# Optimization experiments

Hardware: AMD Instinct MI355X
Metric: run time of the kernel (lower is better)

The kernel has to match this reference:

```python
import jax, jax.numpy as jnp
import numpy as np

S = 2048      # sequence length
D = 2048      # d_model
H = 16        # n_heads
E = 128       # d_head


def setup_inputs() -> dict:
    key = jax.random.key(0)
    kx, kw = jax.random.split(key)
    x = jax.random.normal(kx, (S, D), dtype=jnp.float32)
    # xavier_normal for fan_in=D, fan_out=3*E per head
    std = float(np.sqrt(2.0 / (D + 3 * E)))
    w_qkv = jax.random.normal(kw, (H, D, 3 * E), dtype=jnp.float32) * std
    return {"x": x, "w_qkv": w_qkv}


def reference(x, w_qkv):
    # qkv: [h, s, 3e]
    qkv = jnp.einsum('sd,hde->hse', x, w_qkv)
    q, k, v = jnp.split(qkv, 3, axis=-1)            # each [h, s, e]
    scores = jnp.einsum('hse,hte->hst', q, k) / jnp.sqrt(jnp.asarray(E, x.dtype))
    attn = jax.nn.softmax(scores, axis=-1)          # [h, s, t]
    out = jnp.einsum('hst,hte->hse', attn, v)       # [h, s, e]
    # concat heads: [s, h*e]
    return out.transpose(1, 0, 2).reshape(x.shape[0], -1)
```

## Files before the change

### kernel.cpp

```cpp
#include <hip/hip_runtime.h>

#define SEQ 2048
#define DMODEL 2048
#define NHEAD 16
#define EHEAD 128
#define NE3 384

using short8 = __attribute__((ext_vector_type(8))) short;
using f32x4  = __attribute__((ext_vector_type(4))) float;
using f32x16 = __attribute__((ext_vector_type(16))) float;
using uint4v = __attribute__((ext_vector_type(4))) unsigned int;

__device__ __forceinline__ unsigned short f32_to_bf16(float f) {
    unsigned int u = __float_as_uint(f);
    unsigned int rounding = 0x7fffu + ((u >> 16) & 1u);
    u += rounding;
    return (unsigned short)(u >> 16);
}

__device__ __forceinline__ void async_load16(const void* g, void* l) {
    __builtin_amdgcn_global_load_lds(
        (const __attribute__((address_space(1))) unsigned int*)g,
        (__attribute__((address_space(3))) unsigned int*)l, 16, 0, 0);
}

#define WG_BARRIER()                              \
    do {                                          \
        asm volatile("" ::: "memory");            \
        __builtin_amdgcn_s_barrier();             \
        asm volatile("" ::: "memory");            \
    } while (0)

__global__ void cast_x_kernel(const float* __restrict__ x, unsigned short* __restrict__ xb) {
    int i = (blockIdx.x * blockDim.x + threadIdx.x) * 4;
    float4 v = *(const float4*)(x + i);
    ushort4 o = make_ushort4(f32_to_bf16(v.x), f32_to_bf16(v.y), f32_to_bf16(v.z), f32_to_bf16(v.w));
    *(ushort4*)(xb + i) = o;
}

__global__ void transpose_w_kernel(const float* __restrict__ w, unsigned short* __restrict__ wT) {
    __shared__ float tile[64][65];
    int h  = blockIdx.z;
    int d0 = blockIdx.x * 64;
    int n0 = blockIdx.y * 64;
    int t = threadIdx.x;
    int rr = t >> 4;
    int cc = (t & 15) * 4;
#pragma unroll
    for (int i = 0; i < 4; i++) {
        float4 v = *(const float4*)&w[(size_t)(h * DMODEL + d0 + rr + i * 16) * NE3 + n0 + cc];
        tile[rr + i * 16][cc + 0] = v.x;
        tile[rr + i * 16][cc + 1] = v.y;
        tile[rr + i * 16][cc + 2] = v.z;
        tile[rr + i * 16][cc + 3] = v.w;
    }
    __syncthreads();
#pragma unroll
    for (int i = 0; i < 4; i++) {
        int n = rr + i * 16;
        ushort4 o;
        o.x = f32_to_bf16(tile[cc + 0][n]);
        o.y = f32_to_bf16(tile[cc + 1][n]);
        o.z = f32_to_bf16(tile[cc + 2][n]);
        o.w = f32_to_bf16(tile[cc + 3][n]);
        *(ushort4*)&wT[(size_t)(h * NE3 + n0 + n) * DMODEL + d0 + cc] = o;
    }
}

template <int B, bool STAGE, int VM>
__device__ __forceinline__ void qkv_kstep(
        unsigned short* lds, f32x4 (&acc)[8][4],
        const unsigned short*& sA0, const unsigned short*& sA1,
        const unsigned short*& sB0, const unsigned short*& sB1,
        const int wave, const int aoff, const int boff) {
    constexpr int B3 = (B + 3) & 3;
    const unsigned short* LA = lds + B * 16384 + aoff;
    const unsigned short* LB = lds + B * 16384 + boff;

    short8 a0[4], bb[4];
#pragma unroll
    for (int mf = 0; mf < 4; ++mf) a0[mf] = *(const short8*)(LA + mf * 512);
#pragma unroll
    for (int nf = 0; nf < 4; ++nf) bb[nf] = *(const short8*)(LB + nf * 512);
    if constexpr (STAGE) {
        async_load16(sA0, lds + B3 * 16384 + wave * 512);
        async_load16(sA1, lds + B3 * 16384 + 4096 + wave * 512);
    }
    sA0 += 32; sA1 += 32;
    WG_BARRIER();
    __builtin_amdgcn_s_setprio(1);
#pragma unroll
    for (int mf = 0; mf < 4; ++mf)
#pragma unroll
        for (int nf = 0; nf < 4; ++nf)
            acc[mf][nf] = __builtin_amdgcn_mfma_f32_16x16x32_bf16(a0[mf], bb[nf], acc[mf][nf], 0, 0, 0);
    __builtin_amdgcn_s_setprio(0);
    WG_BARRIER();

    short8 a1[4];
#pragma unroll
    for (int mf = 0; mf < 4; ++mf) a1[mf] = *(const short8*)(LA + (4 + mf) * 512);
    if constexpr (STAGE) {
        async_load16(sB0, lds + B3 * 16384 + 8192 + wave * 512);
        async_load16(sB1, lds + B3 * 16384 + 12288 + wave * 512);
    }
    sB0 += 32; sB1 += 32;
    if constexpr (VM == 8)      asm volatile("s_waitcnt vmcnt(8)" ::: "memory");
    else if constexpr (VM == 4) asm volatile("s_waitcnt vmcnt(4)" ::: "memory");
    else if constexpr (VM == 0) asm volatile("s_waitcnt vmcnt(0)" ::: "memory");
    WG_BARRIER();
    __builtin_amdgcn_s_setprio(1);
#pragma unroll
    for (int mf = 0; mf < 4; ++mf)
#pragma unroll
        for (int nf = 0; nf < 4; ++nf)
            acc[4 + mf][nf] = __builtin_amdgcn_mfma_f32_16x16x32_bf16(a1[mf], bb[nf], acc[4 + mf][nf], 0, 0, 0);
    __builtin_amdgcn_s_setprio(0);
    WG_BARRIER();
}

__global__ __launch_bounds__(512, 2) void qkv_gemm256(
        const unsigned short* __restrict__ A,
        const unsigned short* __restrict__ Bm,
        unsigned short* __restrict__ Q,
        unsigned short* __restrict__ Kb,
        unsigned short* __restrict__ Vt) {
    extern __shared__ __attribute__((aligned(16))) unsigned short lds[];
    const int mb = blockIdx.x, nb = blockIdx.y;
    const int tid = threadIdx.x;
    const int wave = tid >> 6, lane = tid & 63;
    const int r = lane & 15, q = lane >> 4;
    const int wm = wave >> 2, wn = wave & 3;

    const int c0 = tid, c1 = tid + 512;
    const int rr0 = (c0 >> 2) & 15, rr1 = (c1 >> 2) & 15;
    const int r0 = ((c0 >> 6) << 4) + rr0, k0c = ((c0 & 3) ^ (rr0 & 3)) << 3;
    const int r1 = ((c1 >> 6) << 4) + rr1, k1c = ((c1 & 3) ^ (rr1 & 3)) << 3;

    const unsigned short* sA0 = A  + (size_t)(mb * 256 + r0) * DMODEL + k0c;
    const unsigned short* sA1 = A  + (size_t)(mb * 256 + r1) * DMODEL + k1c;
    const unsigned short* sB0 = Bm + (size_t)(nb * 256 + r0) * DMODEL + k0c;
    const unsigned short* sB1 = Bm + (size_t)(nb * 256 + r1) * DMODEL + k1c;

#pragma unroll
    for (int t = 0; t < 3; ++t) {
        async_load16(sA0 + t * 32, lds + t * 16384 + wave * 512);
        async_load16(sA1 + t * 32, lds + t * 16384 + 4096 + wave * 512);
        async_load16(sB0 + t * 32, lds + t * 16384 + 8192 + wave * 512);
        async_load16(sB1 + t * 32, lds + t * 16384 + 12288 + wave * 512);
    }
    sA0 += 96; sA1 += 96; sB0 += 96; sB1 += 96;

    const int qs = q ^ (r & 3);
    const int aoff = wm * 4096 + r * 32 + qs * 8;
    const int boff = 8192 + wn * 2048 + r * 32 + qs * 8;

    f32x4 acc[8][4] = {};
    asm volatile("s_waitcnt vmcnt(8)" ::: "memory");
    WG_BARRIER();

    for (int i = 0; i < 15; ++i) {
        qkv_kstep<0, true, 8>(lds, acc, sA0, sA1, sB0, sB1, wave, aoff, boff);
        qkv_kstep<1, true, 8>(lds, acc, sA0, sA1, sB0, sB1, wave, aoff, boff);
        qkv_kstep<2, true, 8>(lds, acc, sA0, sA1, sB0, sB1, wave, aoff, boff);
        qkv_kstep<3, true, 8>(lds, acc, sA0, sA1, sB0, sB1, wave, aoff, boff);
    }
    qkv_kstep<0, true,  8>(lds, acc, sA0, sA1, sB0, sB1, wave, aoff, boff);
    qkv_kstep<1, false, 4>(lds, acc, sA0, sA1, sB0, sB1, wave, aoff, boff);
    qkv_kstep<2, false, 0>(lds, acc, sA0, sA1, sB0, sB1, wave, aoff, boff);
    qkv_kstep<3, false, -1>(lds, acc, sA0, sA1, sB0, sB1, wave, aoff, boff);

    const int mbase = mb * 256 + wm * 128;
    const int nbase = nb * 256 + wn * 64;
#pragma unroll
    for (int nf = 0; nf < 4; ++nf) {
        const int cb = nbase + nf * 16;
        const int head = cb / 384;
        const int rem = cb - head * 384;
        const int sel = rem >> 7;
        const int e = (rem & 127) + r;
#pragma unroll
        for (int mf = 0; mf < 8; ++mf) {
            const int row0 = mbase + mf * 16 + q * 4;
            const f32x4 v = acc[mf][nf];
            if (sel == 2) {
                ushort4 o;
                o.x = f32_to_bf16(v[0]);
                o.y = f32_to_bf16(v[1]);
                o.z = f32_to_bf16(v[2]);
                o.w = f32_to_bf16(v[3]);
                *(ushort4*)&Vt[((size_t)head * EHEAD + e) * SEQ + row0] = o;
            } else {
                unsigned short* dst = sel ? Kb : Q;
#pragma unroll
                for (int reg = 0; reg < 4; ++reg)
                    dst[((size_t)head * SEQ + row0 + reg) * EHEAD + e] = f32_to_bf16(v[reg]);
            }
        }
    }
}

__global__ __launch_bounds__(256, 2) void flash_attn(
        const unsigned short* __restrict__ Qg,
        const unsigned short* __restrict__ Kg,
        const unsigned short* __restrict__ Vtg,
        float* __restrict__ out) {
    extern __shared__ __attribute__((aligned(16))) unsigned short lds[];
    unsigned short* sQ  = lds;
    unsigned short* sK0 = lds + 8192;
    unsigned short* sV0 = lds + 24576;

    const int tid = threadIdx.x;
    const int wave = tid >> 6, lane = tid & 63;
    const int l31 = lane & 31, q2 = lane >> 5;
    const int wm = wave >> 1, wn = wave & 1;
    const int b = blockIdx.x;
    const int h  = (b & 7) + (((b >> 3) >> 5) << 3);
    const int m0 = ((b >> 3) & 31) * 64;

    const unsigned short* Qh  = Qg  + ((size_t)h * SEQ + m0) * EHEAD;
    const unsigned short* Kh0 = Kg  + (size_t)h * SEQ * EHEAD;
    const unsigned short* Vh  = Vtg + (size_t)h * EHEAD * SEQ;

    const int qkRow = lane >> 4;
    const int qkPos = lane & 15;
    const int vRow  = lane >> 3;
    const int vPos  = lane & 7;

    const unsigned short* gK[4];
    const unsigned short* gV[4];
#pragma unroll
    for (int c = 0; c < 4; c++) {
        int u = wave * 4 + c;
        int row = u * 4 + qkRow;
        int ch = qkPos ^ (row & 7);
        gK[c] = Kh0 + (size_t)row * EHEAD + ch * 8;
        int rv = u * 8 + vRow;
        int cv = vPos ^ (rv & 7);
        gV[c] = Vh + (size_t)rv * SEQ + cv * 8;
        async_load16(Qh + (size_t)row * EHEAD + ch * 8, sQ + u * 512);
        async_load16(gK[c], sK0 + u * 512);
        async_load16(gV[c], sV0 + u * 512);
        gK[c] += 64 * EHEAD;
        gV[c] += 64;
    }
    __syncthreads();

    short8 bq[8];
    {
        const int row = wm * 32 + l31;
#pragma unroll
        for (int kc = 0; kc < 8; kc++) {
            int p = (kc * 2 + q2) ^ (row & 7);
            bq[kc] = *(const short8*)&sQ[row * 128 + p * 8];
        }
    }

    const unsigned short* kp[8];
    const unsigned short* vp[8];
    const int rowA = wn * 32 + l31;
#pragma unroll
    for (int kc = 0; kc < 8; kc++)
        kp[kc] = sK0 + rowA * 128 + (((kc * 2 + q2) ^ (rowA & 7)) * 8);
#pragma unroll
    for (int et = 0; et < 4; et++)
#pragma unroll
        for (int kc2 = 0; kc2 < 2; kc2++) {
            int rowV = et * 32 + l31;
            int cch = wn * 4 + kc2 * 2 + q2;
            vp[et * 2 + kc2] = sV0 + rowV * 64 + ((cch ^ (rowV & 7)) * 8);
        }

    const float c1 = 0.12752405856f;
    f32x16 acc_o[4] = {};
    float l_acc = 0.f;

    auto body = [&](const int cur, const int nxt, bool pref) {
        if (pref) {
#pragma unroll
            for (int c = 0; c < 4; c++) {
                async_load16(gK[c], sK0 + nxt + (wave * 4 + c) * 512);
                gK[c] += 64 * EHEAD;
            }
#pragma unroll
            for (int c = 0; c < 4; c++) {
                async_load16(gV[c], sV0 + nxt + (wave * 4 + c) * 512);
                gV[c] += 64;
            }
        }

        f32x16 st = {};
#pragma unroll
        for (int kc = 0; kc < 8; kc++) {
            short8 ak = *(const short8*)(kp[kc] + cur);
            st = __builtin_amdgcn_mfma_f32_32x32x16_bf16(ak, bq[kc], st, 0, 0, 0);
        }

        unsigned int pk[8];
#pragma unroll
        for (int t = 0; t < 8; t++) {
            float p0 = __builtin_amdgcn_exp2f(st[2 * t] * c1);
            float p1 = __builtin_amdgcn_exp2f(st[2 * t + 1] * c1);
            l_acc += p0 + p1;
            unsigned int u0 = __float_as_uint(p0) + 0x8000u;
            unsigned int u1 = __float_as_uint(p1) + 0x8000u;
            pk[t] = __builtin_amdgcn_perm(u1, u0, 0x07060302u);
        }

        short8 fr[2];
#pragma unroll
        for (int kc2 = 0; kc2 < 2; kc2++) {
            unsigned int a0 = pk[kc2 * 4 + 0], a1 = pk[kc2 * 4 + 1];
            unsigned int a2 = pk[kc2 * 4 + 2], a3 = pk[kc2 * 4 + 3];
            unsigned int s0 = (unsigned int)__shfl_xor((int)a0, 32);
            unsigned int s1 = (unsigned int)__shfl_xor((int)a1, 32);
            unsigned int s2 = (unsigned int)__shfl_xor((int)a2, 32);
            unsigned int s3 = (unsigned int)__shfl_xor((int)a3, 32);
            uint4v t;
            t.x = q2 ? s2 : a0;
            t.y = q2 ? s3 : a1;
            t.z = q2 ? a2 : s0;
            t.w = q2 ? a3 : s1;
            fr[kc2] = __builtin_bit_cast(short8, t);
        }

#pragma unroll
        for (int et = 0; et < 4; et++)
#pragma unroll
            for (int kc2 = 0; kc2 < 2; kc2++) {
                short8 bv = *(const short8*)(vp[et * 2 + kc2] + cur);
                acc_o[et] = __builtin_amdgcn_mfma_f32_32x32x16_bf16(fr[kc2], bv, acc_o[et], 0, 0, 0);
            }
        __syncthreads();
    };

    for (int ip = 0; ip < SEQ / 128; ip++) {
        body(0, 8192, true);
        body(8192, 0, ip != SEQ / 128 - 1);
    }

    l_acc += __shfl_xor(l_acc, 32);

    float* fl = (float*)lds;
#pragma unroll
    for (int et = 0; et < 4; et++) {
        if ((et >> 1) != wn) {
#pragma unroll
            for (int rg = 0; rg < 4; rg++) {
                f32x4 v;
                v[0] = acc_o[et][rg * 4 + 0];
                v[1] = acc_o[et][rg * 4 + 1];
                v[2] = acc_o[et][rg * 4 + 2];
                v[3] = acc_o[et][rg * 4 + 3];
                *(f32x4*)&fl[(size_t)(((wm * 4 + et) * 4 + rg) * 256) + lane * 4] = v;
            }
        }
    }
    fl[8192 + (wm * 2 + wn) * 32 + l31] = l_acc;
    __syncthreads();

    float invq[4][4];
#pragma unroll
    for (int rg = 0; rg < 4; rg++)
#pragma unroll
        for (int i = 0; i < 4; i++) {
            int qy = i + 4 * q2 + 8 * rg;
            float lt = fl[8192 + (wm * 2 + 0) * 32 + qy] + fl[8192 + (wm * 2 + 1) * 32 + qy];
            invq[rg][i] = 1.0f / lt;
        }

#pragma unroll
    for (int et = 0; et < 4; et++) {
        if ((et >> 1) == wn) {
#pragma unroll
            for (int rg = 0; rg < 4; rg++) {
                f32x4 v = *(const f32x4*)&fl[(size_t)(((wm * 4 + et) * 4 + rg) * 256) + lane * 4];
#pragma unroll
                for (int i = 0; i < 4; i++) {
                    int mrow = i + 4 * q2 + 8 * rg;
                    out[(size_t)(m0 + wm * 32 + mrow) * DMODEL + h * EHEAD + et * 32 + l31] =
                        (acc_o[et][rg * 4 + i] + v[i]) * invq[rg][i];
                }
            }
        }
    }
}

extern "C" void kernel_launch(void* const* d_in, const int* in_sizes, int n_in,
                              void* d_out, int out_size, void* d_ws, size_t ws_size,
                              hipStream_t stream) {
    const float* x = (const float*)d_in[0];
    const float* w = (const float*)d_in[1];
    float* out = (float*)d_out;

    char* ws = (char*)d_ws;
    unsigned short* xb = (unsigned short*)(ws);
    unsigned short* wT = (unsigned short*)(ws + 8388608);
    unsigned short* Q  = (unsigned short*)(ws + 33554432);
    unsigned short* Kb = (unsigned short*)(ws + 41943040);
    unsigned short* Vt = (unsigned short*)(ws + 50331648);

    static bool attr_set = false;
    if (!attr_set) {
        hipFuncSetAttribute((const void*)flash_attn,
                            hipFuncAttributeMaxDynamicSharedMemorySize, 81920);
        hipFuncSetAttribute((const void*)qkv_gemm256,
                            hipFuncAttributeMaxDynamicSharedMemorySize, 131072);
        attr_set = true;
    }

    cast_x_kernel<<<SEQ * DMODEL / (256 * 4), 256, 0, stream>>>(x, xb);
    transpose_w_kernel<<<dim3(DMODEL / 64, NE3 / 64, NHEAD), 256, 0, stream>>>(w, wT);
    qkv_gemm256<<<dim3(SEQ / 256, (NHEAD * NE3) / 256), 512, 131072, stream>>>(xb, wT, Q, Kb, Vt);
    flash_attn<<<512, 256, 81920, stream>>>(Q, Kb, Vt, out);
}
```

Baseline: 209.2 us.

## Retile QKV GEMM to 128x384 blocks aligned to one head

Changes the QKV projection GEMM tile from 256x256 to 128 rows by 384 columns, so each block covers exactly one head's Q, K and V columns. The grid grows from 8x24=192 blocks to 16x16=256 blocks, which fills the CUs more evenly. Each wave now computes a 64x96 sub-tile with a 4x6 accumulator, and the A/B reuse pattern and LDS swizzle change to match. Arithmetic intensity per block drops a little, since the tile is less square, and the epilogue head indexing becomes simpler.

```diff
diff --git a/kernel.cpp b/kernel.cpp
--- a/kernel.cpp
+++ b/kernel.cpp
@@ -69,42 +69,43 @@
 
 template <int B, bool STAGE, int VM>
 __device__ __forceinline__ void qkv_kstep(
-        unsigned short* lds, f32x4 (&acc)[8][4],
-        const unsigned short*& sA0, const unsigned short*& sA1,
-        const unsigned short*& sB0, const unsigned short*& sB1,
-        const int wave, const int aoff, const int boff) {
-    constexpr int B3 = (B + 3) & 3;
+        unsigned short* lds, f32x4 (&acc)[4][6],
+        const unsigned short*& p0, const unsigned short*& p1,
+        const unsigned short*& p2, const unsigned short*& p3,
+        const int d0, const int d1, const int d2, const int d3,
+        const int aoff, const int boff) {
+    constexpr int B3 = ((B + 3) & 3) * 16384;
     const unsigned short* LA = lds + B * 16384 + aoff;
     const unsigned short* LB = lds + B * 16384 + boff;
 
-    short8 a0[4], bb[4];
-#pragma unroll
-    for (int mf = 0; mf < 4; ++mf) a0[mf] = *(const short8*)(LA + mf * 512);
-#pragma unroll
-    for (int nf = 0; nf < 4; ++nf) bb[nf] = *(const short8*)(LB + nf * 512);
+    short8 a[4], b0[3];
+#pragma unroll
+    for (int mf = 0; mf < 4; ++mf) a[mf] = *(const short8*)(LA + mf * 512);
+#pragma unroll
+    for (int nf = 0; nf < 3; ++nf) b0[nf] = *(const short8*)(LB + nf * 512);
     if constexpr (STAGE) {
-        async_load16(sA0, lds + B3 * 16384 + wave * 512);
-        async_load16(sA1, lds + B3 * 16384 + 4096 + wave * 512);
-    }
-    sA0 += 32; sA1 += 32;
+        async_load16(p0, lds + B3 + d0);
+        async_load16(p1, lds + B3 + d1);
+    }
+    p0 += 32; p1 += 32;
     WG_BARRIER();
     __builtin_amdgcn_s_setprio(1);
 #pragma unroll
     for (int mf = 0; mf < 4; ++mf)
 #pragma unroll
-        for (int nf = 0; nf < 4; ++nf)
-            acc[mf][nf] = __builtin_amdgcn_mfma_f32_16x16x32_bf16(a0[mf], bb[nf], acc[mf][nf], 0, 0, 0);
+        for (int nf = 0; nf < 3; ++nf)
+            acc[mf][nf] = __builtin_amdgcn_mfma_f32_16x16x32_bf16(a[mf], b0[nf], acc[mf][nf], 0, 0, 0);
     __builtin_amdgcn_s_setprio(0);
     WG_BARRIER();
 
-    short8 a1[4];
-#pragma unroll
-    for (int mf = 0; mf < 4; ++mf) a1[mf] = *(const short8*)(LA + (4 + mf) * 512);
+    short8 b1[3];
+#pragma unroll
+    for (int nf = 0; nf < 3; ++nf) b1[nf] = *(const short8*)(LB + (3 + nf) * 512);
     if constexpr (STAGE) {
-        async_load16(sB0, lds + B3 * 16384 + 8192 + wave * 512);
-        async_load16(sB1, lds + B3 * 16384 + 12288 + wave * 512);
-    }
-    sB0 += 32; sB1 += 32;
+        async_load16(p2, lds + B3 + d2);
+        async_load16(p3, lds + B3 + d3);
+    }
+    p2 += 32; p3 += 32;
     if constexpr (VM == 8)      asm volatile("s_waitcnt vmcnt(8)" ::: "memory");
     else if constexpr (VM == 4) asm volatile("s_waitcnt vmcnt(4)" ::: "memory");
     else if constexpr (VM == 0) asm volatile("s_waitcnt vmcnt(0)" ::: "memory");
@@ -113,13 +114,13 @@
 #pragma unroll
     for (int mf = 0; mf < 4; ++mf)
 #pragma unroll
-        for (int nf = 0; nf < 4; ++nf)
-            acc[4 + mf][nf] = __builtin_amdgcn_mfma_f32_16x16x32_bf16(a1[mf], bb[nf], acc[4 + mf][nf], 0, 0, 0);
+        for (int nf = 0; nf < 3; ++nf)
+            acc[mf][3 + nf] = __builtin_amdgcn_mfma_f32_16x16x32_bf16(a[mf], b1[nf], acc[mf][3 + nf], 0, 0, 0);
     __builtin_amdgcn_s_setprio(0);
     WG_BARRIER();
 }
 
-__global__ __launch_bounds__(512, 2) void qkv_gemm256(
+__global__ __launch_bounds__(512, 2) void qkv_gemm384(
         const unsigned short* __restrict__ A,
         const unsigned short* __restrict__ Bm,
         unsigned short* __restrict__ Q,
@@ -132,55 +133,55 @@
     const int r = lane & 15, q = lane >> 4;
     const int wm = wave >> 2, wn = wave & 3;
 
-    const int c0 = tid, c1 = tid + 512;
-    const int rr0 = (c0 >> 2) & 15, rr1 = (c1 >> 2) & 15;
-    const int r0 = ((c0 >> 6) << 4) + rr0, k0c = ((c0 & 3) ^ (rr0 & 3)) << 3;
-    const int r1 = ((c1 >> 6) << 4) + rr1, k1c = ((c1 & 3) ^ (rr1 & 3)) << 3;
-
-    const unsigned short* sA0 = A  + (size_t)(mb * 256 + r0) * DMODEL + k0c;
-    const unsigned short* sA1 = A  + (size_t)(mb * 256 + r1) * DMODEL + k1c;
-    const unsigned short* sB0 = Bm + (size_t)(nb * 256 + r0) * DMODEL + k0c;
-    const unsigned short* sB1 = Bm + (size_t)(nb * 256 + r1) * DMODEL + k1c;
+    const int rrm  = (tid >> 2) & 15;
+    const int kg   = ((tid & 3) ^ ((rrm >> 1) & 3)) * 8;
+    const int rowA = ((tid >> 6) << 4) + rrm;
+    const unsigned short* p0 = A  + (size_t)(mb * 128 + rowA) * DMODEL + kg;
+    const unsigned short* p1 = Bm + (size_t)(nb * 384 + rowA) * DMODEL + kg;
+    const unsigned short* p2 = p1 + (size_t)128 * DMODEL;
+    const unsigned short* p3 = p1 + (size_t)256 * DMODEL;
+    const int d0 = wave * 512;
+    const int d1 = 4096 + wave * 512;
+    const int d2 = 8192 + wave * 512;
+    const int d3 = 12288 + wave * 512;
 
 #pragma unroll
     for (int t = 0; t < 3; ++t) {
-        async_load16(sA0 + t * 32, lds + t * 16384 + wave * 512);
-        async_load16(sA1 + t * 32, lds + t * 16384 + 4096 + wave * 512);
-        async_load16(sB0 + t * 32, lds + t * 16384 + 8192 + wave * 512);
-        async_load16(sB1 + t * 32, lds + t * 16384 + 12288 + wave * 512);
-    }
-    sA0 += 96; sA1 += 96; sB0 += 96; sB1 += 96;
-
-    const int qs = q ^ (r & 3);
-    const int aoff = wm * 4096 + r * 32 + qs * 8;
-    const int boff = 8192 + wn * 2048 + r * 32 + qs * 8;
-
-    f32x4 acc[8][4] = {};
+        async_load16(p0 + t * 32, lds + t * 16384 + d0);
+        async_load16(p1 + t * 32, lds + t * 16384 + d1);
+        async_load16(p2 + t * 32, lds + t * 16384 + d2);
+        async_load16(p3 + t * 32, lds + t * 16384 + d3);
+    }
+    p0 += 96; p1 += 96; p2 += 96; p3 += 96;
+
+    const int qs = q ^ ((r >> 1) & 3);
+    const int aoff = wm * 2048 + r * 32 + qs * 8;
+    const int boff = 4096 + wn * 3072 + r * 32 + qs * 8;
+
+    f32x4 acc[4][6] = {};
     asm volatile("s_waitcnt vmcnt(8)" ::: "memory");
     WG_BARRIER();
 
     for (int i = 0; i < 15; ++i) {
-        qkv_kstep<0, true, 8>(lds, acc, sA0, sA1, sB0, sB1, wave, aoff, boff);
-        qkv_kstep<1, true, 8>(lds, acc, sA0, sA1, sB0, sB1, wave, aoff, boff);
-        qkv_kstep<2, true, 8>(lds, acc, sA0, sA1, sB0, sB1, wave, aoff, boff);
-        qkv_kstep<3, true, 8>(lds, acc, sA0, sA1, sB0, sB1, wave, aoff, boff);
-    }
-    qkv_kstep<0, true,  8>(lds, acc, sA0, sA1, sB0, sB1, wave, aoff, boff);
-    qkv_kstep<1, false, 4>(lds, acc, sA0, sA1, sB0, sB1, wave, aoff, boff);
-    qkv_kstep<2, false, 0>(lds, acc, sA0, sA1, sB0, sB1, wave, aoff, boff);
-    qkv_kstep<3, false, -1>(lds, acc, sA0, sA1, sB0, sB1, wave, aoff, boff);
-
-    const int mbase = mb * 256 + wm * 128;
-    const int nbase = nb * 256 + wn * 64;
-#pragma unroll
-    for (int nf = 0; nf < 4; ++nf) {
-        const int cb = nbase + nf * 16;
-        const int head = cb / 384;
-        const int rem = cb - head * 384;
-        const int sel = rem >> 7;
-        const int e = (rem & 127) + r;
-#pragma unroll
-        for (int mf = 0; mf < 8; ++mf) {
+        qkv_kstep<0, true, 8>(lds, acc, p0, p1, p2, p3, d0, d1, d2, d3, aoff, boff);
+        qkv_kstep<1, true, 8>(lds, acc, p0, p1, p2, p3, d0, d1, d2, d3, aoff, boff);
+        qkv_kstep<2, true, 8>(lds, acc, p0, p1, p2, p3, d0, d1, d2, d3, aoff, boff);
+        qkv_kstep<3, true, 8>(lds, acc, p0, p1, p2, p3, d0, d1, d2, d3, aoff, boff);
+    }
+    qkv_kstep<0, true,  8>(lds, acc, p0, p1, p2, p3, d0, d1, d2, d3, aoff, boff);
+    qkv_kstep<1, false, 4>(lds, acc, p0, p1, p2, p3, d0, d1, d2, d3, aoff, boff);
+    qkv_kstep<2, false, 0>(lds, acc, p0, p1, p2, p3, d0, d1, d2, d3, aoff, boff);
+    qkv_kstep<3, false, -1>(lds, acc, p0, p1, p2, p3, d0, d1, d2, d3, aoff, boff);
+
+    const int head = nb;
+    const int mbase = mb * 128 + wm * 64;
+#pragma unroll
+    for (int nf = 0; nf < 6; ++nf) {
+        const int cb = wn * 96 + nf * 16;
+        const int sel = cb >> 7;
+        const int e = (cb & 127) + r;
+#pragma unroll
+        for (int mf = 0; mf < 4; ++mf) {
             const int row0 = mbase + mf * 16 + q * 4;
             const f32x4 v = acc[mf][nf];
             if (sel == 2) {
@@ -404,13 +405,13 @@
     if (!attr_set) {
         hipFuncSetAttribute((const void*)flash_attn,
                             hipFuncAttributeMaxDynamicSharedMemorySize, 81920);
-        hipFuncSetAttribute((const void*)qkv_gemm256,
+        hipFuncSetAttribute((const void*)qkv_gemm384,
                             hipFuncAttributeMaxDynamicSharedMemorySize, 131072);
         attr_set = true;
     }
 
     cast_x_kernel<<<SEQ * DMODEL / (256 * 4), 256, 0, stream>>>(x, xb);
     transpose_w_kernel<<<dim3(DMODEL / 64, NE3 / 64, NHEAD), 256, 0, stream>>>(w, wT);
-    qkv_gemm256<<<dim3(SEQ / 256, (NHEAD * NE3) / 256), 512, 131072, stream>>>(xb, wT, Q, Kb, Vt);
+    qkv_gemm384<<<dim3(SEQ / 128, NHEAD), 512, 131072, stream>>>(xb, wT, Q, Kb, Vt);
     flash_attn<<<512, 256, 81920, stream>>>(Q, Kb, Vt, out);
 }
```

Result: faster. 202.8 us (-3.1%).
